# Performance work log

Hardware: AMD Instinct MI355X
Metric: run time of the kernel (lower is better)

## Reference

```python
import jax, jax.numpy as jnp
import numpy as np

N, E, C, A, R = 8192, 65536, 64, 16, 8
DIMS = (1, 3, 5, 7)        # dims of l = 0..3 irrep blocks
IRDIM = sum(DIMS)          # 16
L = len(DIMS)              # 4 TP paths (0e x l -> l, 'uvu')
WN = L * C                 # conv_tp weight_numel = 256
HID = 64                   # radial MLP hidden width
AVG_NUM_NEIGH = 16.0


def setup_inputs() -> dict:
    key = jax.random.key(0)
    ks = jax.random.split(key, 18)
    f = lambda k, s: jax.random.normal(k, s, dtype=jnp.float32)
    return dict(
        node_attrs=f(ks[0], (N, A)),
        node_feats=f(ks[1], (N, C)),
        edge_attrs=f(ks[2], (E, IRDIM)),
        edge_feats=f(ks[3], (E, R)),
        edge_index=jax.random.randint(ks[4], (2, E), 0, N),
        magmom_node_inv_feats=f(ks[5], (N, R)),
        magmom_node_attrs=f(ks[6], (N, IRDIM)),
        # learned parameters (e3nn-style, no biases, 1/sqrt(fan_in) path norm)
        W_up=f(ks[7], (C, C)),
        W_r0=f(ks[8], (R + R, HID)),
        W_r1=f(ks[9], (HID, HID)),
        W_r2=f(ks[10], (HID, HID)),
        W_r3=f(ks[11], (HID, WN)),
        W_trans=f(ks[12], (WN, WN)),
        W_dens=f(ks[13], (R, 1)),
        W_lin=f(ks[14], (L, C, C)),
        W_mlin=f(ks[15], (L, C, C)),
        W_skip=f(ks[16], (L, C, A, C)),
        W_mskip=f(ks[17], (L, C, A, C)),
    )


def _per_l_linear(x, W):
    # equivariant Linear: independent channel-mixing per l block. x: [N,C,16]
    outs, o = [], 0
    for l, d in enumerate(DIMS):
        outs.append(jnp.einsum('ncm,cd->ndm', x[:, :, o:o + d], W[l]) / np.sqrt(C))
        o += d
    return jnp.concatenate(outs, axis=-1)


def _skip_tp(x, attrs, W):
    # FullyConnectedTensorProduct with scalar (0e) node attrs: (l x 0e -> l, 'uvw')
    outs, o = [], 0
    for l, d in enumerate(DIMS):
        outs.append(jnp.einsum('num,nv,uvw->nwm', x[:, :, o:o + d], attrs, W[l]) / np.sqrt(C * A))
        o += d
    return jnp.concatenate(outs, axis=-1)


def _weighted_tp(xj, attrs_e, w):
    # weighted TP of 0e node feats with lmax=3 attrs: per-edge 'uvu' weights.
    # xj: [E,C], attrs_e: [E,16], w: [E,L,C] -> [E,C,16]
    wf = jnp.repeat(w, np.array(DIMS), axis=1, total_repeat_length=IRDIM)  # [E,16,C]
    return xj[:, :, None] * attrs_e[:, None, :] * jnp.swapaxes(wf, 1, 2)


def reference(node_attrs, node_feats, edge_attrs, edge_feats, edge_index,
              magmom_node_inv_feats, magmom_node_attrs,
              W_up, W_r0, W_r1, W_r2, W_r3, W_trans, W_dens,
              W_lin, W_mlin, W_skip, W_mskip):
    sender, receiver = edge_index[0], edge_index[1]
    x = node_feats @ W_up / np.sqrt(C)                     # linear_up (0e)
    xj = x[sender]                                         # gather by sender
    h = jnp.concatenate([edge_feats, magmom_node_inv_feats[sender]], axis=-1)
    for W in (W_r0, W_r1, W_r2):                           # radial MLP (silu)
        h = jax.nn.silu(h @ W / np.sqrt(W.shape[0]))
    tp_w = (h @ W_r3 / np.sqrt(HID)).reshape(E, L, C)      # per-edge TP weights
    edge_density = jnp.tanh((edge_feats @ W_dens / np.sqrt(R)) ** 2)  # [E,1]
    mji = _weighted_tp(xj, edge_attrs, tp_w)               # [E,C,16]
    tp_w_m = (tp_w.reshape(E, WN) @ W_trans / np.sqrt(WN)).reshape(E, L, C)
    magmom_mji = _weighted_tp(xj, magmom_node_attrs[sender], tp_w_m)
    density = jax.ops.segment_sum(edge_density, receiver, num_segments=N)       # [N,1]
    message = jax.ops.segment_sum(mji, receiver, num_segments=N)                # [N,C,16]
    magmom_message = jax.ops.segment_sum(magmom_mji, receiver, num_segments=N)
    message = _per_l_linear(message, W_lin) / (density[:, :, None] + 1.0)
    message = _skip_tp(message, node_attrs, W_skip)
    magmom_message = _per_l_linear(magmom_message, W_mlin) / AVG_NUM_NEIGH
    magmom_message = _skip_tp(magmom_message, node_attrs, W_mskip)
    return message, magmom_message                         # each [N,C,16] (reshape_irreps layout)
```

## Files before the change

kernel.cpp:

```cpp
#include <hip/hip_runtime.h>

#define N_NODES 8192
#define N_EDGES 65536

typedef __attribute__((ext_vector_type(8))) short bf16x8;
typedef __attribute__((ext_vector_type(4))) float f32x4;

static __device__ __forceinline__ float bfl(unsigned v){ unsigned u=v<<16; float f; __builtin_memcpy(&f,&u,4); return f; }
static __device__ __forceinline__ float bfh(unsigned v){ unsigned u=v&0xffff0000u; float f; __builtin_memcpy(&f,&u,4); return f; }
static __device__ __forceinline__ float bfs(unsigned short h){ unsigned u=((unsigned)h)<<16; float f; __builtin_memcpy(&f,&u,4); return f; }
static __device__ __forceinline__ unsigned short f2bf(float f){ unsigned u; __builtin_memcpy(&u,&f,4); u += 0x7fffu + ((u>>16)&1u); return (unsigned short)(u>>16); }
static __device__ __forceinline__ unsigned pk(float a, float b){ return (unsigned)f2bf(a) | ((unsigned)f2bf(b)<<16); }
static __device__ __forceinline__ float silu_f(float v){ return v/(1.f+__expf(-v)); }

__global__ __launch_bounds__(256) void k_linup(const float* __restrict__ nf,
                                               const float* __restrict__ wup,
                                               float* __restrict__ x){
    __shared__ float s[4][64];
    const int t=threadIdx.x, wv=t>>6, lane=t&63;
    const int n=blockIdx.x*4+wv;
    s[wv][lane]=nf[(size_t)n*64+lane];
    __syncthreads();
    float acc=0.f;
    for(int c=0;c<64;++c) acc += s[wv][c]*wup[c*64+lane];
    x[(size_t)n*64+lane]=acc*0.125f;
}

__global__ __launch_bounds__(256) void k_wmlp(const float* __restrict__ wr0,
                                              const float* __restrict__ wr1,
                                              const float* __restrict__ wr2,
                                              unsigned short* __restrict__ w0f,
                                              unsigned short* __restrict__ w1f,
                                              unsigned short* __restrict__ w2f){
    const int b=blockIdx.x, t=threadIdx.x;
    #pragma unroll
    for(int z=0;z<2;++z){
        int idx=t*2+z;
        int lane=idx>>3, i=idx&7;
        if(b<4){
            int nt=b, k=(lane>>4)*8+i, n=nt*16+(lane&15);
            float v=(k<16)? wr0[k*64+n]*0.25f : 0.f;
            w0f[(nt*64+lane)*8+i]=f2bf(v);
        } else if(b<12){
            int q=b-4, nt=q>>1, ks=q&1;
            int k=ks*32+(lane>>4)*8+i, n=nt*16+(lane&15);
            w1f[((nt*2+ks)*64+lane)*8+i]=f2bf(wr1[k*64+n]*0.125f);
        } else {
            int q=b-12, nt=q>>1, ks=q&1;
            int k=ks*32+(lane>>4)*8+i, n=nt*16+(lane&15);
            w2f[((nt*2+ks)*64+lane)*8+i]=f2bf(wr2[k*64+n]*0.125f);
        }
    }
}

__global__ __launch_bounds__(256) void k_wtf(const float* __restrict__ wr3,
                                             const float* __restrict__ wtr,
                                             unsigned short* __restrict__ wtf){
    const int b=blockIdx.x;
    const int mt=b>>1, ks=b&1, t=threadIdx.x;
    #pragma unroll
    for(int z=0;z<2;++z){
        int idx=t*2+z;
        int lane=idx>>3, i=idx&7;
        int k=ks*32+(lane>>4)*8+i;
        int n=mt*16+(lane&15);
        int j=n>>3, s=n&7;
        float v;
        if(s<4) v=wr3[k*256+s*64+j]*0.125f;
        else {
            float acc=0.f;
            for(int kk=0;kk<256;++kk) acc+=wr3[k*256+kk]*wtr[kk*256+(s-4)*64+j];
            v=acc*(1.f/128.f);
        }
        wtf[((size_t)b*64+lane)*8+i]=f2bf(v);
    }
}

__global__ __launch_bounds__(256) void k_wwf(const float* __restrict__ wlin,
                                             const float* __restrict__ wmlin,
                                             const float* __restrict__ wskip,
                                             const float* __restrict__ wmskip,
                                             unsigned* __restrict__ wwf){
    const int b=blockIdx.x, ten=b>>8, lc=b&255, l=lc>>6, c=lc&63;
    const float* WL = ten? wmlin:wlin;
    const float* WS = ten? wmskip:wskip;
    const float scale = ten? (1.f/4096.f):(1.f/256.f);
    const int t=threadIdx.x, wg=t>>6, s=t&63, lane=s>>1, half=s&1;
    const int kg=lane>>4, w=wg*16+(lane&15);
    const int v0=kg*8+half*4;
    float a0=0,a1=0,a2=0,a3=0;
    for(int u=0;u<64;++u){
        float wl=WL[(l*64+c)*64+u];
        const float* wsp=&WS[(((l*64+u)*16+v0)*64)+w];
        a0+=wl*wsp[0]; a1+=wl*wsp[64]; a2+=wl*wsp[128]; a3+=wl*wsp[192];
    }
    size_t fi=(((size_t)ten*4+l)*64+c)*4+wg;
    unsigned* op=wwf + (fi*32+lane)*4 + half*2;
    op[0]=pk(a0*scale,a1*scale); op[1]=pk(a2*scale,a3*scale);
}

__global__ __launch_bounds__(256) void k_count(const int* __restrict__ recv, int* __restrict__ cnt){
    int e=blockIdx.x*256+threadIdx.x;
    atomicAdd(&cnt[recv[e]],1);
}
__global__ __launch_bounds__(1024) void k_scan(const int* __restrict__ cnt, int* __restrict__ rowptr, int* __restrict__ cur){
    __shared__ int s[1024];
    const int t=threadIdx.x;
    int c[8]; int sum=0;
    #pragma unroll
    for(int i=0;i<8;++i){ c[i]=cnt[t*8+i]; sum+=c[i]; }
    s[t]=sum; __syncthreads();
    for(int off=1;off<1024;off<<=1){
        int v=s[t]; int add=(t>=off)? s[t-off]:0;
        __syncthreads();
        s[t]=v+add;
        __syncthreads();
    }
    int run=s[t]-sum;
    #pragma unroll
    for(int i=0;i<8;++i){ rowptr[t*8+i]=run; cur[t*8+i]=run; run+=c[i]; }
    if(t==1023) rowptr[8192]=run;
}
__global__ __launch_bounds__(256) void k_scatter(const int* __restrict__ recv, int* __restrict__ cur, int* __restrict__ elist){
    int e=blockIdx.x*256+threadIdx.x;
    int r=recv[e];
    int p=atomicAdd(&cur[r],1);
    elist[p]=e;
}

__global__ __launch_bounds__(256) void k_edge2(
    const float* __restrict__ ef, const float* __restrict__ mminv,
    const float* __restrict__ mattr, const int* __restrict__ sender,
    const float* __restrict__ wdens,
    const uint4* __restrict__ w0f, const uint4* __restrict__ w1f,
    const uint4* __restrict__ w2f, const uint4* __restrict__ wtf,
    const float* __restrict__ x,
    unsigned short* __restrict__ wxc, float* __restrict__ man, float* __restrict__ ed)
{
    __shared__ unsigned short hA[4096];
    __shared__ unsigned short hB[4096];
    __shared__ float xs[64*68];
    const int t=threadIdx.x, lane=t&63, wv=t>>6;
    const int tile=blockIdx.x*64;

    {
        const int e=t>>2, q=t&3, ge=tile+e;
        const int s=sender[ge];
        const float4* xp=(const float4*)(x+(size_t)s*64+q*16);
        float4* xw=(float4*)&xs[e*68+q*16];
        xw[0]=xp[0]; xw[1]=xp[1]; xw[2]=xp[2]; xw[3]=xp[3];
        *(float4*)(man+(size_t)ge*16+q*4) = *(const float4*)(mattr+(size_t)s*16+q*4);
        const int se3=(e&7)<<3;
        if(q==0){
            float4 f0=*(const float4*)(ef+(size_t)ge*8);
            float4 f1=*(const float4*)(ef+(size_t)ge*8+4);
            uint4 o; o.x=pk(f0.x,f0.y); o.y=pk(f0.z,f0.w); o.z=pk(f1.x,f1.y); o.w=pk(f1.z,f1.w);
            *(uint4*)&hA[e*64 + (0^se3)]=o;
            float acc=f0.x*wdens[0]+f0.y*wdens[1]+f0.z*wdens[2]+f0.w*wdens[3]
                     +f1.x*wdens[4]+f1.y*wdens[5]+f1.z*wdens[6]+f1.w*wdens[7];
            acc*=0.35355339059327373f;
            float q2=acc*acc;
            float ex=__expf(2.f*q2);
            ed[ge]=1.f-2.f/(ex+1.f);
        } else if(q==1){
            float4 f0=*(const float4*)(mminv+(size_t)s*8);
            float4 f1=*(const float4*)(mminv+(size_t)s*8+4);
            uint4 o; o.x=pk(f0.x,f0.y); o.y=pk(f0.z,f0.w); o.z=pk(f1.x,f1.y); o.w=pk(f1.z,f1.w);
            *(uint4*)&hA[e*64 + (8^se3)]=o;
        } else if(q==2){
            *(uint4*)&hA[e*64 + (16^se3)]=make_uint4(0,0,0,0);
        } else {
            *(uint4*)&hA[e*64 + (24^se3)]=make_uint4(0,0,0,0);
        }
    }
    __syncthreads();

    const int arow=wv*16+(lane&15);
    const int akg=lane>>4;
    const int aswz=(arow&7)<<3;
    const int dcol=lane&15;
    const int drow0=wv*16+(lane>>4)*4;

    {
        uint4 av=*(const uint4*)&hA[arow*64+((akg*8)^aswz)];
        bf16x8 a; __builtin_memcpy(&a,&av,16);
        f32x4 d[4];
        #pragma unroll
        for(int nt=0;nt<4;++nt){
            uint4 bw=w0f[nt*64+lane];
            bf16x8 b; __builtin_memcpy(&b,&bw,16);
            f32x4 z={0.f,0.f,0.f,0.f};
            d[nt]=__builtin_amdgcn_mfma_f32_16x16x32_bf16(a,b,z,0,0,0);
        }
        #pragma unroll
        for(int nt=0;nt<4;++nt){
            #pragma unroll
            for(int r=0;r<4;++r){
                int e2=drow0+r, n=nt*16+dcol;
                hB[e2*64 + (n^((e2&7)<<3))]=f2bf(silu_f(d[nt][r]));
            }
        }
    }
    __syncthreads();

    {
        uint4 av0=*(const uint4*)&hB[arow*64+(((0+akg)*8)^aswz)];
        uint4 av1=*(const uint4*)&hB[arow*64+(((4+akg)*8)^aswz)];
        bf16x8 a0,a1; __builtin_memcpy(&a0,&av0,16); __builtin_memcpy(&a1,&av1,16);
        f32x4 d[4];
        #pragma unroll
        for(int nt=0;nt<4;++nt){
            uint4 bw0=w1f[(nt*2+0)*64+lane];
            uint4 bw1=w1f[(nt*2+1)*64+lane];
            bf16x8 b0,b1; __builtin_memcpy(&b0,&bw0,16); __builtin_memcpy(&b1,&bw1,16);
            f32x4 z={0.f,0.f,0.f,0.f};
            d[nt]=__builtin_amdgcn_mfma_f32_16x16x32_bf16(a0,b0,z,0,0,0);
            d[nt]=__builtin_amdgcn_mfma_f32_16x16x32_bf16(a1,b1,d[nt],0,0,0);
        }
        #pragma unroll
        for(int nt=0;nt<4;++nt){
            #pragma unroll
            for(int r=0;r<4;++r){
                int e2=drow0+r, n=nt*16+dcol;
                hA[e2*64 + (n^((e2&7)<<3))]=f2bf(silu_f(d[nt][r]));
            }
        }
    }
    __syncthreads();

    {
        uint4 av0=*(const uint4*)&hA[arow*64+(((0+akg)*8)^aswz)];
        uint4 av1=*(const uint4*)&hA[arow*64+(((4+akg)*8)^aswz)];
        bf16x8 a0,a1; __builtin_memcpy(&a0,&av0,16); __builtin_memcpy(&a1,&av1,16);
        f32x4 d[4];
        #pragma unroll
        for(int nt=0;nt<4;++nt){
            uint4 bw0=w2f[(nt*2+0)*64+lane];
            uint4 bw1=w2f[(nt*2+1)*64+lane];
            bf16x8 b0,b1; __builtin_memcpy(&b0,&bw0,16); __builtin_memcpy(&b1,&bw1,16);
            f32x4 z={0.f,0.f,0.f,0.f};
            d[nt]=__builtin_amdgcn_mfma_f32_16x16x32_bf16(a0,b0,z,0,0,0);
            d[nt]=__builtin_amdgcn_mfma_f32_16x16x32_bf16(a1,b1,d[nt],0,0,0);
        }
        #pragma unroll
        for(int nt=0;nt<4;++nt){
            #pragma unroll
            for(int r=0;r<4;++r){
                int e2=drow0+r, n=nt*16+dcol;
                hB[e2*64 + (n^((e2&7)<<3))]=f2bf(silu_f(d[nt][r]));
            }
        }
    }
    __syncthreads();

    {
        bf16x8 hb[4][2];
        #pragma unroll
        for(int nt2=0;nt2<4;++nt2){
            int erow=nt2*16+(lane&15);
            int esz=(erow&7)<<3;
            #pragma unroll
            for(int ks=0;ks<2;++ks){
                uint4 v=*(const uint4*)&hB[erow*64+(((ks*4+akg)*8)^esz)];
                __builtin_memcpy(&hb[nt2][ks],&v,16);
            }
        }
        const int g=lane>>4;
        const int jo=g>>1, sh=g&1;
        for(int mt=0;mt<8;++mt){
            int mtg=wv*8+mt;
            uint4 aw0=wtf[(mtg*2+0)*64+lane];
            uint4 aw1=wtf[(mtg*2+1)*64+lane];
            bf16x8 a0,a1; __builtin_memcpy(&a0,&aw0,16); __builtin_memcpy(&a1,&aw1,16);
            int j=mtg*2+jo;
            #pragma unroll
            for(int nt2=0;nt2<4;++nt2){
                f32x4 z={0.f,0.f,0.f,0.f};
                f32x4 d=__builtin_amdgcn_mfma_f32_16x16x32_bf16(a0,hb[nt2][0],z,0,0,0);
                d=__builtin_amdgcn_mfma_f32_16x16x32_bf16(a1,hb[nt2][1],d,0,0,0);
                int eloc=nt2*16+(lane&15);
                float xj=xs[eloc*68+j];
                uint2 o; o.x=pk(d[0]*xj,d[1]*xj); o.y=pk(d[2]*xj,d[3]*xj);
                *(uint2*)&wxc[((size_t)(tile+eloc)*64+j)*8+sh*4]=o;
            }
        }
    }
}

__global__ __launch_bounds__(256) void k_gather(
    const int* __restrict__ rowptr, const int* __restrict__ elist,
    const unsigned short* __restrict__ wxc, const float* __restrict__ ea,
    const float* __restrict__ man, const float* __restrict__ ed,
    float* __restrict__ out)
{
    const int t=threadIdx.x, wv=t>>6, lane=t&63;
    const int n=blockIdx.x*4+wv;
    const int r0=rowptr[n], r1=rowptr[n+1];
    float msg[16]; float mm[16];
    #pragma unroll
    for(int m=0;m<16;++m){ msg[m]=0.f; mm[m]=0.f; }
    float dens=0.f;
    for(int k=r0;k<r1;++k){
        int e=elist[k];
        uint4 r=*(const uint4*)(wxc+((size_t)e*64+lane)*8);
        float wx0=bfl(r.x),wx1=bfh(r.x),wx2=bfl(r.y),wx3=bfh(r.y);
        float wm0=bfl(r.z),wm1=bfh(r.z),wm2=bfl(r.w),wm3=bfh(r.w);
        dens+=ed[e];
        const float4* eap=(const float4*)(ea+(size_t)e*16);
        const float4* map=(const float4*)(man+(size_t)e*16);
        float4 A0=eap[0],A1=eap[1],A2=eap[2],A3=eap[3];
        float4 B0=map[0],B1=map[1],B2=map[2],B3=map[3];
        msg[0]+=wx0*A0.x;
        msg[1]+=wx1*A0.y;  msg[2]+=wx1*A0.z;  msg[3]+=wx1*A0.w;
        msg[4]+=wx2*A1.x;  msg[5]+=wx2*A1.y;  msg[6]+=wx2*A1.z;  msg[7]+=wx2*A1.w;  msg[8]+=wx2*A2.x;
        msg[9]+=wx3*A2.y;  msg[10]+=wx3*A2.z; msg[11]+=wx3*A2.w;
        msg[12]+=wx3*A3.x; msg[13]+=wx3*A3.y; msg[14]+=wx3*A3.z; msg[15]+=wx3*A3.w;
        mm[0]+=wm0*B0.x;
        mm[1]+=wm1*B0.y;  mm[2]+=wm1*B0.z;  mm[3]+=wm1*B0.w;
        mm[4]+=wm2*B1.x;  mm[5]+=wm2*B1.y;  mm[6]+=wm2*B1.z;  mm[7]+=wm2*B1.w;  mm[8]+=wm2*B2.x;
        mm[9]+=wm3*B2.y;  mm[10]+=wm3*B2.z; mm[11]+=wm3*B2.w;
        mm[12]+=wm3*B3.x; mm[13]+=wm3*B3.y; mm[14]+=wm3*B3.z; mm[15]+=wm3*B3.w;
    }
    float inv=1.f/(1.f+dens);
    float* mp=out+(size_t)n*1024+lane*16;
    ((float4*)mp)[0]=make_float4(msg[0]*inv,msg[1]*inv,msg[2]*inv,msg[3]*inv);
    ((float4*)mp)[1]=make_float4(msg[4]*inv,msg[5]*inv,msg[6]*inv,msg[7]*inv);
    ((float4*)mp)[2]=make_float4(msg[8]*inv,msg[9]*inv,msg[10]*inv,msg[11]*inv);
    ((float4*)mp)[3]=make_float4(msg[12]*inv,msg[13]*inv,msg[14]*inv,msg[15]*inv);
    float* qp=out+8388608+(size_t)n*1024+lane*16;
    ((float4*)qp)[0]=make_float4(mm[0],mm[1],mm[2],mm[3]);
    ((float4*)qp)[1]=make_float4(mm[4],mm[5],mm[6],mm[7]);
    ((float4*)qp)[2]=make_float4(mm[8],mm[9],mm[10],mm[11]);
    ((float4*)qp)[3]=make_float4(mm[12],mm[13],mm[14],mm[15]);
}

__global__ __launch_bounds__(256) void k_final7(const float* __restrict__ attrs,
                                                const unsigned* __restrict__ wwf,
                                                float* __restrict__ out){
    __shared__ unsigned short msgS[64*16*8];
    const int blk=blockIdx.x;
    const int half=blk&1;
    const int rest=blk>>1;
    const int ten=rest>>9, nb=(rest&511)*16;
    float* base=out+(size_t)ten*8388608;
    const int t=threadIdx.x, lane=t&63, wg=t>>6;

    const float4* src=(const float4*)(base+(size_t)nb*1024);
    #pragma unroll
    for(int i=0;i<8;++i){
        int tau=i*256+t;
        int n=tau>>7, rem=tau&127, c=rem>>1, qq=rem&1;
        float4 f=src[(n<<8)+(c<<2)+half*2+qq];
        unsigned* dst=(unsigned*)&msgS[(c*16+n)*8+qq*4];
        dst[0]=pk(f.x,f.y); dst[1]=pk(f.z,f.w);
    }
    bf16x8 afrag;
    {
        int nloc=lane&15, kg=lane>>4;
        if(kg<2){
            const float* ap=attrs+(size_t)(nb+nloc)*16+kg*8;
            #pragma unroll
            for(int i=0;i<8;++i) afrag[i]=(short)f2bf(ap[i]);
        } else {
            #pragma unroll
            for(int i=0;i<8;++i) afrag[i]=0;
        }
    }
    __syncthreads();

    const int g4=(lane>>4)*4;
    const int colw=lane&15;
    float acc[4][8];
    #pragma unroll
    for(int r=0;r<4;++r)
        #pragma unroll
        for(int m=0;m<8;++m) acc[r][m]=0.f;

    const uint4* wwf4=(const uint4*)wwf;
    const int l31=lane&31;

    if(half==0){
        const uint4* p0=wwf4+((size_t)((ten*4+0)*64)*4+wg)*32+l31;
        const uint4* p1=wwf4+((size_t)((ten*4+1)*64)*4+wg)*32+l31;
        const uint4* p2=wwf4+((size_t)((ten*4+2)*64)*4+wg)*32+l31;
        uint4 b0=p0[0], b1=p1[0], b2=p2[0];
        for(int c=0;c<64;++c){
            uint4 n0,n1,n2;
            if(c<63){ n0=p0[(c+1)*128]; n1=p1[(c+1)*128]; n2=p2[(c+1)*128]; }
            bf16x8 f0,f1,f2;
            __builtin_memcpy(&f0,&b0,16); __builtin_memcpy(&f1,&b1,16); __builtin_memcpy(&f2,&b2,16);
            f32x4 z={0.f,0.f,0.f,0.f};
            f32x4 d0=__builtin_amdgcn_mfma_f32_16x16x32_bf16(afrag,f0,z,0,0,0);
            f32x4 d1=__builtin_amdgcn_mfma_f32_16x16x32_bf16(afrag,f1,z,0,0,0);
            f32x4 d2=__builtin_amdgcn_mfma_f32_16x16x32_bf16(afrag,f2,z,0,0,0);
            #pragma unroll
            for(int r=0;r<4;++r){
                uint4 h=*(const uint4*)&msgS[(c*16+g4+r)*8];
                float dr0=d0[r], dr1=d1[r], dr2=d2[r];
                acc[r][0]+=bfl(h.x)*dr0;
                acc[r][1]+=bfh(h.x)*dr1;
                acc[r][2]+=bfl(h.y)*dr1;
                acc[r][3]+=bfh(h.y)*dr1;
                acc[r][4]+=bfl(h.z)*dr2;
                acc[r][5]+=bfh(h.z)*dr2;
                acc[r][6]+=bfl(h.w)*dr2;
                acc[r][7]+=bfh(h.w)*dr2;
            }
            if(c<63){ b0=n0; b1=n1; b2=n2; }
        }
    } else {
        const uint4* p0=wwf4+((size_t)((ten*4+2)*64)*4+wg)*32+l31;
        const uint4* p1=wwf4+((size_t)((ten*4+3)*64)*4+wg)*32+l31;
        uint4 b0=p0[0], b1=p1[0];
        for(int c=0;c<64;++c){
            uint4 n0,n1;
            if(c<63){ n0=p0[(c+1)*128]; n1=p1[(c+1)*128]; }
            bf16x8 f0,f1;
            __builtin_memcpy(&f0,&b0,16); __builtin_memcpy(&f1,&b1,16);
            f32x4 z={0.f,0.f,0.f,0.f};
            f32x4 d0=__builtin_amdgcn_mfma_f32_16x16x32_bf16(afrag,f0,z,0,0,0);
            f32x4 d1=__builtin_amdgcn_mfma_f32_16x16x32_bf16(afrag,f1,z,0,0,0);
            #pragma unroll
            for(int r=0;r<4;++r){
                uint4 h=*(const uint4*)&msgS[(c*16+g4+r)*8];
                float dr0=d0[r], dr1=d1[r];
                acc[r][0]+=bfl(h.x)*dr0;
                acc[r][1]+=bfh(h.x)*dr1;
                acc[r][2]+=bfl(h.y)*dr1;
                acc[r][3]+=bfh(h.y)*dr1;
                acc[r][4]+=bfl(h.z)*dr1;
                acc[r][5]+=bfh(h.z)*dr1;
                acc[r][6]+=bfl(h.w)*dr1;
                acc[r][7]+=bfh(h.w)*dr1;
            }
            if(c<63){ b0=n0; b1=n1; }
        }
    }
    const int w=wg*16+colw;
    #pragma unroll
    for(int r=0;r<4;++r){
        float* op=base+(size_t)(nb+g4+r)*1024+w*16+half*8;
        ((float4*)op)[0]=make_float4(acc[r][0],acc[r][1],acc[r][2],acc[r][3]);
        ((float4*)op)[1]=make_float4(acc[r][4],acc[r][5],acc[r][6],acc[r][7]);
    }
}

extern "C" void kernel_launch(void* const* d_in, const int* in_sizes, int n_in,
                              void* d_out, int out_size, void* d_ws, size_t ws_size,
                              hipStream_t stream) {
    const float* node_attrs=(const float*)d_in[0];
    const float* node_feats=(const float*)d_in[1];
    const float* edge_attrs=(const float*)d_in[2];
    const float* edge_feats=(const float*)d_in[3];
    const int*   eidx_in  =(const int*)  d_in[4];
    const int*   sender   =eidx_in;
    const int*   recv     =eidx_in+N_EDGES;
    const float* mminv    =(const float*)d_in[5];
    const float* mattr    =(const float*)d_in[6];
    const float* wup      =(const float*)d_in[7];
    const float* wr0      =(const float*)d_in[8];
    const float* wr1      =(const float*)d_in[9];
    const float* wr2      =(const float*)d_in[10];
    const float* wr3      =(const float*)d_in[11];
    const float* wtr      =(const float*)d_in[12];
    const float* wdens    =(const float*)d_in[13];
    const float* wlin     =(const float*)d_in[14];
    const float* wmlin    =(const float*)d_in[15];
    const float* wskip    =(const float*)d_in[16];
    const float* wmskip   =(const float*)d_in[17];

    char* ws=(char*)d_ws;
    float*          x     =(float*)(ws+0);
    unsigned short* wxc   =(unsigned short*)(ws+2097152);
    float*          man   =(float*)(ws+69206016);
    float*          ed    =(float*)(ws+73400320);
    unsigned short* wtf   =(unsigned short*)(ws+73662464);
    unsigned*       wwf   =(unsigned*)(ws+73728000);
    unsigned short* w0f   =(unsigned short*)(ws+75825152);
    unsigned short* w1f   =(unsigned short*)(ws+75829248);
    unsigned short* w2f   =(unsigned short*)(ws+75837440);
    int*            cnt   =(int*)(ws+75845632);
    int*            rowptr=(int*)(ws+75878400);
    int*            cur   =(int*)(ws+75911296);
    int*            elist =(int*)(ws+75944064);
    if(ws_size < (size_t)76206208) return;

    float* out=(float*)d_out;

    hipMemsetAsync(cnt,0,32768,stream);
    k_linup  <<<dim3(2048),dim3(256),0,stream>>>(node_feats,wup,x);
    k_wmlp   <<<dim3(20),  dim3(256),0,stream>>>(wr0,wr1,wr2,w0f,w1f,w2f);
    k_wtf    <<<dim3(64),  dim3(256),0,stream>>>(wr3,wtr,wtf);
    k_wwf    <<<dim3(512), dim3(256),0,stream>>>(wlin,wmlin,wskip,wmskip,wwf);
    k_count  <<<dim3(256), dim3(256),0,stream>>>(recv,cnt);
    k_scan   <<<dim3(1),   dim3(1024),0,stream>>>(cnt,rowptr,cur);
    k_scatter<<<dim3(256), dim3(256),0,stream>>>(recv,cur,elist);
    k_edge2  <<<dim3(1024),dim3(256),0,stream>>>(edge_feats,mminv,mattr,sender,wdens,
                                                 (const uint4*)w0f,(const uint4*)w1f,
                                                 (const uint4*)w2f,(const uint4*)wtf,
                                                 x,wxc,man,ed);
    k_gather <<<dim3(2048),dim3(256),0,stream>>>(rowptr,elist,wxc,edge_attrs,man,ed,out);
    k_final7 <<<dim3(2048),dim3(256),0,stream>>>(node_attrs,wwf,out);
}
```

Before: 250.5 us.

## Fuse gather with final linear/skip TP, split wxc layout, precompute W_r3·W_trans

```diff
diff --git a/kernel.cpp b/kernel.cpp
--- a/kernel.cpp
+++ b/kernel.cpp
@@ -53,8 +53,17 @@
     }
 }
 
+__global__ __launch_bounds__(256) void k_w3t(const float* __restrict__ wr3,
+                                             const float* __restrict__ wtr,
+                                             float* __restrict__ wt){
+    const int k=blockIdx.x, n=threadIdx.x;
+    float acc=0.f;
+    for(int kk=0;kk<256;++kk) acc += wr3[k*256+kk]*wtr[kk*256+n];
+    wt[k*256+n]=acc;
+}
+
 __global__ __launch_bounds__(256) void k_wtf(const float* __restrict__ wr3,
-                                             const float* __restrict__ wtr,
+                                             const float* __restrict__ wt,
                                              unsigned short* __restrict__ wtf){
     const int b=blockIdx.x;
     const int mt=b>>1, ks=b&1, t=threadIdx.x;
@@ -65,13 +74,8 @@
         int k=ks*32+(lane>>4)*8+i;
         int n=mt*16+(lane&15);
         int j=n>>3, s=n&7;
-        float v;
-        if(s<4) v=wr3[k*256+s*64+j]*0.125f;
-        else {
-            float acc=0.f;
-            for(int kk=0;kk<256;++kk) acc+=wr3[k*256+kk]*wtr[kk*256+(s-4)*64+j];
-            v=acc*(1.f/128.f);
-        }
+        float v = (s<4)? wr3[k*256+s*64+j]*0.125f
+                       : wt[k*256+(s-4)*64+j]*(1.f/128.f);
         wtf[((size_t)b*64+lane)*8+i]=f2bf(v);
     }
 }
@@ -130,12 +134,12 @@
 
 __global__ __launch_bounds__(256) void k_edge2(
     const float* __restrict__ ef, const float* __restrict__ mminv,
-    const float* __restrict__ mattr, const int* __restrict__ sender,
+    const int* __restrict__ sender,
     const float* __restrict__ wdens,
     const uint4* __restrict__ w0f, const uint4* __restrict__ w1f,
     const uint4* __restrict__ w2f, const uint4* __restrict__ wtf,
     const float* __restrict__ x,
-    unsigned short* __restrict__ wxc, float* __restrict__ man, float* __restrict__ ed)
+    unsigned short* __restrict__ wxc, float* __restrict__ ed)
 {
     __shared__ unsigned short hA[4096];
     __shared__ unsigned short hB[4096];
@@ -149,7 +153,6 @@
         const float4* xp=(const float4*)(x+(size_t)s*64+q*16);
         float4* xw=(float4*)&xs[e*68+q*16];
         xw[0]=xp[0]; xw[1]=xp[1]; xw[2]=xp[2]; xw[3]=xp[3];
-        *(float4*)(man+(size_t)ge*16+q*4) = *(const float4*)(mattr+(size_t)s*16+q*4);
         const int se3=(e&7)<<3;
         if(q==0){
             float4 f0=*(const float4*)(ef+(size_t)ge*8);
@@ -281,79 +284,69 @@
                 int eloc=nt2*16+(lane&15);
                 float xj=xs[eloc*68+j];
                 uint2 o; o.x=pk(d[0]*xj,d[1]*xj); o.y=pk(d[2]*xj,d[3]*xj);
-                *(uint2*)&wxc[((size_t)(tile+eloc)*64+j)*8+sh*4]=o;
-            }
-        }
-    }
-}
-
-__global__ __launch_bounds__(256) void k_gather(
+                *(uint2*)&wxc[(size_t)sh*16777216 + ((size_t)(tile+eloc)*64+j)*4]=o;
+            }
+        }
+    }
+}
+
+__global__ __launch_bounds__(256) void k_gf2(
     const int* __restrict__ rowptr, const int* __restrict__ elist,
-    const unsigned short* __restrict__ wxc, const float* __restrict__ ea,
-    const float* __restrict__ man, const float* __restrict__ ed,
+    const int* __restrict__ sender,
+    const unsigned short* __restrict__ wxc,
+    const float* __restrict__ ea, const float* __restrict__ mattr,
+    const float* __restrict__ ed,
+    const float* __restrict__ attrs, const unsigned* __restrict__ wwf,
     float* __restrict__ out)
 {
-    const int t=threadIdx.x, wv=t>>6, lane=t&63;
-    const int n=blockIdx.x*4+wv;
-    const int r0=rowptr[n], r1=rowptr[n+1];
-    float msg[16]; float mm[16];
-    #pragma unroll
-    for(int m=0;m<16;++m){ msg[m]=0.f; mm[m]=0.f; }
-    float dens=0.f;
-    for(int k=r0;k<r1;++k){
-        int e=elist[k];
-        uint4 r=*(const uint4*)(wxc+((size_t)e*64+lane)*8);
-        float wx0=bfl(r.x),wx1=bfh(r.x),wx2=bfl(r.y),wx3=bfh(r.y);
-        float wm0=bfl(r.z),wm1=bfh(r.z),wm2=bfl(r.w),wm3=bfh(r.w);
-        dens+=ed[e];
-        const float4* eap=(const float4*)(ea+(size_t)e*16);
-        const float4* map=(const float4*)(man+(size_t)e*16);
-        float4 A0=eap[0],A1=eap[1],A2=eap[2],A3=eap[3];
-        float4 B0=map[0],B1=map[1],B2=map[2],B3=map[3];
-        msg[0]+=wx0*A0.x;
-        msg[1]+=wx1*A0.y;  msg[2]+=wx1*A0.z;  msg[3]+=wx1*A0.w;
-        msg[4]+=wx2*A1.x;  msg[5]+=wx2*A1.y;  msg[6]+=wx2*A1.z;  msg[7]+=wx2*A1.w;  msg[8]+=wx2*A2.x;
-        msg[9]+=wx3*A2.y;  msg[10]+=wx3*A2.z; msg[11]+=wx3*A2.w;
-        msg[12]+=wx3*A3.x; msg[13]+=wx3*A3.y; msg[14]+=wx3*A3.z; msg[15]+=wx3*A3.w;
-        mm[0]+=wm0*B0.x;
-        mm[1]+=wm1*B0.y;  mm[2]+=wm1*B0.z;  mm[3]+=wm1*B0.w;
-        mm[4]+=wm2*B1.x;  mm[5]+=wm2*B1.y;  mm[6]+=wm2*B1.z;  mm[7]+=wm2*B1.w;  mm[8]+=wm2*B2.x;
-        mm[9]+=wm3*B2.y;  mm[10]+=wm3*B2.z; mm[11]+=wm3*B2.w;
-        mm[12]+=wm3*B3.x; mm[13]+=wm3*B3.y; mm[14]+=wm3*B3.z; mm[15]+=wm3*B3.w;
-    }
-    float inv=1.f/(1.f+dens);
-    float* mp=out+(size_t)n*1024+lane*16;
-    ((float4*)mp)[0]=make_float4(msg[0]*inv,msg[1]*inv,msg[2]*inv,msg[3]*inv);
-    ((float4*)mp)[1]=make_float4(msg[4]*inv,msg[5]*inv,msg[6]*inv,msg[7]*inv);
-    ((float4*)mp)[2]=make_float4(msg[8]*inv,msg[9]*inv,msg[10]*inv,msg[11]*inv);
-    ((float4*)mp)[3]=make_float4(msg[12]*inv,msg[13]*inv,msg[14]*inv,msg[15]*inv);
-    float* qp=out+8388608+(size_t)n*1024+lane*16;
-    ((float4*)qp)[0]=make_float4(mm[0],mm[1],mm[2],mm[3]);
-    ((float4*)qp)[1]=make_float4(mm[4],mm[5],mm[6],mm[7]);
-    ((float4*)qp)[2]=make_float4(mm[8],mm[9],mm[10],mm[11]);
-    ((float4*)qp)[3]=make_float4(mm[12],mm[13],mm[14],mm[15]);
-}
-
-__global__ __launch_bounds__(256) void k_final7(const float* __restrict__ attrs,
-                                                const unsigned* __restrict__ wwf,
-                                                float* __restrict__ out){
     __shared__ unsigned short msgS[64*16*8];
     const int blk=blockIdx.x;
     const int half=blk&1;
     const int rest=blk>>1;
     const int ten=rest>>9, nb=(rest&511)*16;
-    float* base=out+(size_t)ten*8388608;
-    const int t=threadIdx.x, lane=t&63, wg=t>>6;
-
-    const float4* src=(const float4*)(base+(size_t)nb*1024);
-    #pragma unroll
-    for(int i=0;i<8;++i){
-        int tau=i*256+t;
-        int n=tau>>7, rem=tau&127, c=rem>>1, qq=rem&1;
-        float4 f=src[(n<<8)+(c<<2)+half*2+qq];
-        unsigned* dst=(unsigned*)&msgS[(c*16+n)*8+qq*4];
-        dst[0]=pk(f.x,f.y); dst[1]=pk(f.z,f.w);
-    }
+    const int t=threadIdx.x, lane=t&63, wv=t>>6;
+
+    const unsigned short* wbase = wxc + (size_t)ten*16777216;
+    for(int nn=0;nn<4;++nn){
+        const int n=nb+wv*4+nn;
+        const int r0=rowptr[n], r1=rowptr[n+1];
+        float msg[8];
+        #pragma unroll
+        for(int m=0;m<8;++m) msg[m]=0.f;
+        float dens=0.f;
+        if(half==0){
+            for(int k=r0;k<r1;++k){
+                int e=elist[k];
+                uint2 v=*(const uint2*)&wbase[(size_t)e*256+lane*4];
+                const float4* ap;
+                if(ten==0){ dens+=ed[e]; ap=(const float4*)(ea+(size_t)e*16); }
+                else      { int s=sender[e]; ap=(const float4*)(mattr+(size_t)s*16); }
+                float4 A0=ap[0],A1=ap[1];
+                float wx0=bfl(v.x),wx1=bfh(v.x),wx2=bfl(v.y);
+                msg[0]+=wx0*A0.x; msg[1]+=wx1*A0.y; msg[2]+=wx1*A0.z; msg[3]+=wx1*A0.w;
+                msg[4]+=wx2*A1.x; msg[5]+=wx2*A1.y; msg[6]+=wx2*A1.z; msg[7]+=wx2*A1.w;
+            }
+        } else {
+            for(int k=r0;k<r1;++k){
+                int e=elist[k];
+                uint2 v=*(const uint2*)&wbase[(size_t)e*256+lane*4];
+                const float4* ap;
+                if(ten==0){ dens+=ed[e]; ap=(const float4*)(ea+(size_t)e*16); }
+                else      { int s=sender[e]; ap=(const float4*)(mattr+(size_t)s*16); }
+                float4 A2=ap[2],A3=ap[3];
+                float wx2=bfl(v.y),wx3=bfh(v.y);
+                msg[0]+=wx2*A2.x; msg[1]+=wx3*A2.y; msg[2]+=wx3*A2.z; msg[3]+=wx3*A2.w;
+                msg[4]+=wx3*A3.x; msg[5]+=wx3*A3.y; msg[6]+=wx3*A3.z; msg[7]+=wx3*A3.w;
+            }
+        }
+        const float inv = ten? 1.f : 1.f/(1.f+dens);
+        const int np=(wv*4+nn)^(lane&15);
+        uint4 o;
+        o.x=pk(msg[0]*inv,msg[1]*inv); o.y=pk(msg[2]*inv,msg[3]*inv);
+        o.z=pk(msg[4]*inv,msg[5]*inv); o.w=pk(msg[6]*inv,msg[7]*inv);
+        *(uint4*)&msgS[((size_t)lane*16+np)*8]=o;
+    }
+
     bf16x8 afrag;
     {
         int nloc=lane&15, kg=lane>>4;
@@ -370,6 +363,7 @@
 
     const int g4=(lane>>4)*4;
     const int colw=lane&15;
+    const int wg=wv;
     float acc[4][8];
     #pragma unroll
     for(int r=0;r<4;++r)
@@ -393,9 +387,11 @@
             f32x4 d0=__builtin_amdgcn_mfma_f32_16x16x32_bf16(afrag,f0,z,0,0,0);
             f32x4 d1=__builtin_amdgcn_mfma_f32_16x16x32_bf16(afrag,f1,z,0,0,0);
             f32x4 d2=__builtin_amdgcn_mfma_f32_16x16x32_bf16(afrag,f2,z,0,0,0);
+            const int cm=c&15;
             #pragma unroll
             for(int r=0;r<4;++r){
-                uint4 h=*(const uint4*)&msgS[(c*16+g4+r)*8];
+                const int np=(g4+r)^cm;
+                uint4 h=*(const uint4*)&msgS[((size_t)c*16+np)*8];
                 float dr0=d0[r], dr1=d1[r], dr2=d2[r];
                 acc[r][0]+=bfl(h.x)*dr0;
                 acc[r][1]+=bfh(h.x)*dr1;
@@ -420,9 +416,11 @@
             f32x4 z={0.f,0.f,0.f,0.f};
             f32x4 d0=__builtin_amdgcn_mfma_f32_16x16x32_bf16(afrag,f0,z,0,0,0);
             f32x4 d1=__builtin_amdgcn_mfma_f32_16x16x32_bf16(afrag,f1,z,0,0,0);
+            const int cm=c&15;
             #pragma unroll
             for(int r=0;r<4;++r){
-                uint4 h=*(const uint4*)&msgS[(c*16+g4+r)*8];
+                const int np=(g4+r)^cm;
+                uint4 h=*(const uint4*)&msgS[((size_t)c*16+np)*8];
                 float dr0=d0[r], dr1=d1[r];
                 acc[r][0]+=bfl(h.x)*dr0;
                 acc[r][1]+=bfh(h.x)*dr1;
@@ -436,6 +434,8 @@
             if(c<63){ b0=n0; b1=n1; }
         }
     }
+
+    float* base=out+(size_t)ten*8388608;
     const int w=wg*16+colw;
     #pragma unroll
     for(int r=0;r<4;++r){
@@ -472,7 +472,7 @@
     char* ws=(char*)d_ws;
     float*          x     =(float*)(ws+0);
     unsigned short* wxc   =(unsigned short*)(ws+2097152);
-    float*          man   =(float*)(ws+69206016);
+    float*          wt    =(float*)(ws+69206016);
     float*          ed    =(float*)(ws+73400320);
     unsigned short* wtf   =(unsigned short*)(ws+73662464);
     unsigned*       wwf   =(unsigned*)(ws+73728000);
@@ -490,15 +490,16 @@
     hipMemsetAsync(cnt,0,32768,stream);
     k_linup  <<<dim3(2048),dim3(256),0,stream>>>(node_feats,wup,x);
     k_wmlp   <<<dim3(20),  dim3(256),0,stream>>>(wr0,wr1,wr2,w0f,w1f,w2f);
-    k_wtf    <<<dim3(64),  dim3(256),0,stream>>>(wr3,wtr,wtf);
+    k_w3t    <<<dim3(64),  dim3(256),0,stream>>>(wr3,wtr,wt);
+    k_wtf    <<<dim3(64),  dim3(256),0,stream>>>(wr3,wt,wtf);
     k_wwf    <<<dim3(512), dim3(256),0,stream>>>(wlin,wmlin,wskip,wmskip,wwf);
     k_count  <<<dim3(256), dim3(256),0,stream>>>(recv,cnt);
     k_scan   <<<dim3(1),   dim3(1024),0,stream>>>(cnt,rowptr,cur);
     k_scatter<<<dim3(256), dim3(256),0,stream>>>(recv,cur,elist);
-    k_edge2  <<<dim3(1024),dim3(256),0,stream>>>(edge_feats,mminv,mattr,sender,wdens,
+    k_edge2  <<<dim3(1024),dim3(256),0,stream>>>(edge_feats,mminv,sender,wdens,
                                                  (const uint4*)w0f,(const uint4*)w1f,
                                                  (const uint4*)w2f,(const uint4*)wtf,
-                                                 x,wxc,man,ed);
-    k_gather <<<dim3(2048),dim3(256),0,stream>>>(rowptr,elist,wxc,edge_attrs,man,ed,out);
-    k_final7 <<<dim3(2048),dim3(256),0,stream>>>(node_attrs,wwf,out);
-}
+                                                 x,wxc,ed);
+    k_gf2    <<<dim3(2048),dim3(256),0,stream>>>(rowptr,elist,sender,wxc,
+                                                 edge_attrs,mattr,ed,node_attrs,wwf,out);
+}
```

Result: slower. 271.7 us (+8.5%).
